# Performance work log

Measured on AMD Instinct MI355X. Metric: run time of the kernel, lower is better.

## Reference

```python
import jax, jax.numpy as jnp
import numpy as np
from jax import lax

FIELD = 32          # backbone receptive-field stride (field_size of ResNet50)
K = 3               # number of anchor sizes
ANCHOR_PX = (32, 64, 96)
POOL = 2
TILES = 3
NMS_IOU = 0.3
R_POST = 512        # post-NMS proposal cap (static shape for jit)
IMG = 1536
MG = IMG // FIELD   # 48x48 feature map
C = 256
HID = 1024


def setup_inputs() -> dict:
    key = jax.random.key(0)
    ks = jax.random.split(key, 6)
    # create_anchors: per feature cell (grid step FIELD) and per anchor size,
    # row = [x_upper_left, y_upper_left, width, height]
    grid = np.arange(MG, dtype=np.float32) * FIELD + FIELD / 2.0  # cell centers
    cy, cx, aa = np.meshgrid(grid, grid, np.array(ANCHOR_PX, np.float32), indexing='ij')
    anchors = np.stack([cx - aa / 2, cy - aa / 2, aa, aa], axis=-1).reshape(-1, 4).astype(np.float32)
    return {
        'features': jax.random.normal(ks[0], (1, MG, MG, C), jnp.float32),
        'anchors': jnp.asarray(anchors),
        'W_obj': jax.random.normal(ks[1], (C, 2 * K), jnp.float32) * 0.1,
        'b_obj': jnp.zeros((2 * K,), jnp.float32),
        'W_reg': jax.random.normal(ks[2], (C, 4 * K), jnp.float32) * 0.01,
        'b_reg': jnp.zeros((4 * K,), jnp.float32),
        'W_fc1': jax.random.normal(ks[3], (TILES * TILES * C, HID), jnp.float32) * 0.02,
        'b_fc1': jnp.zeros((HID,), jnp.float32),
        'W_fc2': jax.random.normal(ks[4], (HID, 4), jnp.float32) * 0.01,
        'b_fc2': jnp.zeros((4,), jnp.float32),
    }


def _map_outputs(out, anchors):
    # out: [M, N, K*D] RPN output; returns [A, D], one row per anchor
    apx = jnp.asarray(ANCHOR_PX, jnp.int32)
    k = jnp.argmax(anchors[:, 3].astype(jnp.int32)[:, None] == apx[None, :], axis=1)
    px = ((anchors[:, 0] + anchors[:, 2] * 0.5) / FIELD).astype(jnp.int32)
    py = ((anchors[:, 1] + anchors[:, 3] * 0.5) / FIELD).astype(jnp.int32)
    M, N, _ = out.shape
    r = out.reshape(M, N, K, -1)
    return r[py, px, k]


def _unparameterize(reg, anchors):
    cxa = anchors[:, 0] + anchors[:, 2] * 0.5
    cya = anchors[:, 1] + anchors[:, 3] * 0.5
    cx = reg[:, 0] * anchors[:, 2] + cxa
    cy = reg[:, 1] * anchors[:, 3] + cya
    w = anchors[:, 2] * jnp.exp(reg[:, 2])
    h = anchors[:, 3] * jnp.exp(reg[:, 3])
    return jnp.stack([cx - w * 0.5, cy - h * 0.5, w, h], axis=1)


def _clip_boxes(b, W, H):
    x1 = jnp.clip(b[:, 0], 0.0, W)
    y1 = jnp.clip(b[:, 1], 0.0, H)
    x2 = jnp.clip(b[:, 0] + b[:, 2], 0.0, W)
    y2 = jnp.clip(b[:, 1] + b[:, 3], 0.0, H)
    return jnp.stack([x1, y1, x2 - x1, y2 - y1], axis=1)


def _pairwise_iou(b):
    x1, y1 = b[:, 0], b[:, 1]
    x2, y2 = b[:, 0] + b[:, 2], b[:, 1] + b[:, 3]
    iw = jnp.maximum(0.0, jnp.minimum(x2[:, None], x2[None, :]) - jnp.maximum(x1[:, None], x1[None, :]))
    ih = jnp.maximum(0.0, jnp.minimum(y2[:, None], y2[None, :]) - jnp.maximum(y1[:, None], y1[None, :]))
    inter = iw * ih
    area = (x2 - x1) * (y2 - y1)
    return inter / (area[:, None] + area[None, :] - inter + 1e-8)


def _roialign(fmap, boxes):
    # fmap: [M, N, C]; boxes: [R, 4] xywh -> [R, TILES, TILES, C]
    M, N, Cc = fmap.shape
    S = TILES * POOL
    offs = (jnp.arange(S, dtype=boxes.dtype) + 0.5) / S
    fx = jnp.clip((boxes[:, 0:1] + offs[None, :] * boxes[:, 2:3]) / FIELD - 0.5, 0.0, N - 1.0)
    fy = jnp.clip((boxes[:, 1:2] + offs[None, :] * boxes[:, 3:4]) / FIELD - 0.5, 0.0, M - 1.0)
    x0 = jnp.floor(fx).astype(jnp.int32); x1 = jnp.minimum(x0 + 1, N - 1); wx = fx - x0
    y0 = jnp.floor(fy).astype(jnp.int32); y1 = jnp.minimum(y0 + 1, M - 1); wy = fy - y0
    def g(yi, xi):
        return fmap[yi[:, :, None], xi[:, None, :]]  # [R, S, S, C]
    wX = wx[:, None, :, None]; wY = wy[:, :, None, None]
    v = (g(y0, x0) * (1 - wY) * (1 - wX) + g(y0, x1) * (1 - wY) * wX
         + g(y1, x0) * wY * (1 - wX) + g(y1, x1) * wY * wX)
    R = boxes.shape[0]
    return v.reshape(R, TILES, POOL, TILES, POOL, Cc).mean(axis=(2, 4))


def reference(features, anchors, W_obj, b_obj, W_reg, b_reg, W_fc1, b_fc1, W_fc2, b_fc2):
    fmap = features[0]  # [M, N, C]
    out_obj = fmap @ W_obj + b_obj   # [M, N, 2K]
    out_reg = fmap @ W_reg + b_reg   # [M, N, 4K]
    rpn_obj = jax.nn.softmax(_map_outputs(out_obj, anchors), axis=1)  # [A, 2]
    rpn_reg = _map_outputs(out_reg, anchors)                          # [A, 4]
    boxes = _clip_boxes(_unparameterize(rpn_reg, anchors), float(IMG), float(IMG))
    scores = rpn_obj[:, 1]
    A = boxes.shape[0]
    # NMS (sequential greedy suppression on score-sorted boxes)
    order = jnp.argsort(-scores)
    iou_mat = lax.stop_gradient(_pairwise_iou(boxes[order]))  # [A, A], index selection is non-diff
    idx = jnp.arange(A)
    def body(i, keep):
        sup = jnp.any((iou_mat[i] > NMS_IOU) & keep & (idx < i))
        return keep.at[i].set(~sup)
    keep = lax.fori_loop(0, A, body, jnp.zeros((A,), bool))
    masked = jnp.where(keep, scores[order], -1e9)
    _, topi = lax.top_k(masked, R_POST)
    sel = order[topi]
    sel_boxes = boxes[sel]
    sel_obj = rpn_obj[sel]
    pooled = _roialign(fmap, sel_boxes)            # [R, TILES, TILES, C]
    flat = pooled.reshape(R_POST, -1)
    h = jax.nn.relu(flat @ W_fc1 + b_fc1)
    align_reg = h @ W_fc2 + b_fc2                  # [R, 4]
    align_boxes = _unparameterize(align_reg, sel_boxes)
    # concat (rpn_obj, rpn_boxes, align_boxes) -> [R, 10]
    return jnp.concatenate([sel_obj, sel_boxes, align_boxes], axis=1)
```

## Files before the change

### kernel.cpp

```cpp
#include <hip/hip_runtime.h>
#include <hip/hip_bf16.h>

typedef unsigned long long ull;

#define MGRID 48
#define CCH   256
#define NCELL 2304
#define NA    6912
#define NW    108
#define NHID  1024
#define KFC   2304
#define RPOST 512
#define IMGF  1536.0f

typedef __attribute__((ext_vector_type(8))) short short8v;
typedef __attribute__((ext_vector_type(4))) float f32x4;

__global__ __launch_bounds__(256) void rpn_wcvt(const float* __restrict__ feat,
    const float* __restrict__ Wobj, const float* __restrict__ bobj,
    const float* __restrict__ Wreg, const float* __restrict__ breg,
    float* __restrict__ rpn, const float* __restrict__ Wfc1,
    ushort* __restrict__ Wt){
  if (blockIdx.x >= 162){
    __shared__ float tile[32][33];
    int bid = blockIdx.x - 162;
    int bx = bid & 31;
    int by = bid >> 5;
    int tx = threadIdx.x & 31, ty = threadIdx.x >> 5;
    #pragma unroll
    for (int it=0; it<4; ++it)
      tile[ty + 8*it][tx] = Wfc1[(size_t)(by*32 + ty + 8*it)*NHID + bx*32 + tx];
    __syncthreads();
    #pragma unroll
    for (int it=0; it<4; ++it){
      __hip_bfloat16 b = __float2bfloat16(tile[tx][ty + 8*it]);
      Wt[(size_t)(bx*32 + ty + 8*it)*KFC + by*32 + tx] = *(ushort*)&b;
    }
    return;
  }
  int g = blockIdx.x*256 + threadIdx.x;
  int cell = g / 18, o = g % 18;
  const float* W; int stride; float acc;
  if (o < 6){ W = Wobj + o; stride = 6;  acc = bobj[o];   }
  else      { W = Wreg + (o-6); stride = 12; acc = breg[o-6]; }
  const float4* x4 = (const float4*)(feat + cell*CCH);
  #pragma unroll 4
  for (int c4=0;c4<CCH/4;++c4){
    float4 xv = x4[c4];
    acc += xv.x*W[(4*c4+0)*stride];
    acc += xv.y*W[(4*c4+1)*stride];
    acc += xv.z*W[(4*c4+2)*stride];
    acc += xv.w*W[(4*c4+3)*stride];
  }
  rpn[cell*18 + o] = acc;
}

__global__ __launch_bounds__(256) void anchor_prep(const float* __restrict__ rpn,
    const float* __restrict__ anchors, float* __restrict__ probs,
    float* __restrict__ boxes, ull* __restrict__ keys){
  int a = blockIdx.x*256 + threadIdx.x;
  int cell = a/3, k = a%3;
  const float* rc = rpn + cell*18;
  float l0 = rc[2*k], l1 = rc[2*k+1];
  float m  = fmaxf(l0,l1);
  float e0 = expf(l0-m), e1 = expf(l1-m);
  float s  = e0 + e1;
  float p0 = e0/s, p1 = e1/s;
  probs[a*2+0] = p0; probs[a*2+1] = p1;
  float4 an = ((const float4*)anchors)[a];
  float r0 = rc[6+4*k+0], r1 = rc[6+4*k+1], r2 = rc[6+4*k+2], r3 = rc[6+4*k+3];
  float cxa = an.x + an.z*0.5f, cya = an.y + an.w*0.5f;
  float cx = r0*an.z + cxa, cy = r1*an.w + cya;
  float w  = an.z*expf(r2),  hh = an.w*expf(r3);
  float bx = cx - w*0.5f, by = cy - hh*0.5f;
  float x1 = fminf(fmaxf(bx,      0.0f), IMGF);
  float y1 = fminf(fmaxf(by,      0.0f), IMGF);
  float x2 = fminf(fmaxf(bx + w,  0.0f), IMGF);
  float y2 = fminf(fmaxf(by + hh, 0.0f), IMGF);
  float4 bo; bo.x = x1; bo.y = y1; bo.z = x2 - x1; bo.w = y2 - y1;
  ((float4*)boxes)[a] = bo;
  keys[a] = ((ull)__float_as_uint(p1) << 32) | (unsigned)(NA-1-a);
}

__global__ __launch_bounds__(256) void rank_part(const ull* __restrict__ keys,
                                                 int* __restrict__ part){
  __shared__ ull lk[256];
  int t = threadIdx.x;
  int ib = blockIdx.x, jb = blockIdx.y;
  lk[t] = keys[jb*256 + t];
  int i = ib*256 + t;
  ull ki = keys[i];
  __syncthreads();
  int cnt = 0;
  #pragma unroll 16
  for (int j=0;j<256;++j) cnt += (lk[j] > ki) ? 1 : 0;
  part[jb*NA + i] = cnt;
}

__global__ __launch_bounds__(256) void rank_scatter(const int* __restrict__ part,
    const float* __restrict__ boxes, int* __restrict__ ord, float* __restrict__ sboxes){
  int i = blockIdx.x*256 + threadIdx.x;
  int r = 0;
  #pragma unroll
  for (int jb=0;jb<27;++jb) r += part[jb*NA + i];
  ord[r] = i;
  ((float4*)sboxes)[r] = ((const float4*)boxes)[i];
}

#define NQ 5993
__global__ __launch_bounds__(256) void iou_mask(const float* __restrict__ sboxes,
                                                ull* __restrict__ maskT){
  int g = blockIdx.x*256 + threadIdx.x;
  int q = g >> 6;
  if (q >= NQ) return;
  int w = (int)((sqrtf(8.0f*(float)q + 9.0f) - 3.0f) * 0.5f);
  if (w > 107) w = 107;
  while (w < 107 && (w+1)*(w+4)/2 <= q) ++w;
  while (w > 0 && w*(w+3)/2 > q) --w;
  int ib = q - w*(w+3)/2;
  int i = ib*64 + (g & 63);
  float4 bi = ((const float4*)sboxes)[i];
  float x1i = bi.x, y1i = bi.y;
  float x2i = bi.x + bi.z, y2i = bi.y + bi.w;
  float ai  = (x2i - x1i) * (y2i - y1i);
  const float4* bj4 = (const float4*)sboxes + w*64;
  ull bits = 0;
  #pragma unroll 8
  for (int jj=0;jj<64;++jj){
    float4 bj = bj4[jj];
    float x1j = bj.x, y1j = bj.y;
    float x2j = bj.x + bj.z, y2j = bj.y + bj.w;
    float aj  = (x2j - x1j) * (y2j - y1j);
    float iw = fmaxf(fminf(x2i,x2j) - fmaxf(x1i,x1j), 0.0f);
    float ih = fmaxf(fminf(y2i,y2j) - fmaxf(y1i,y1j), 0.0f);
    float inter = iw*ih;
    float den = ai + aj - inter + 1e-8f;
    if (inter > 0.3f*den) bits |= (1ull<<jj);
  }
  maskT[(size_t)w*NA + i] = bits;
}

__global__ __launch_bounds__(256) void nms(const ull* __restrict__ maskT,
    const int* __restrict__ ord, const float* __restrict__ sboxes,
    const float* __restrict__ probs, float* __restrict__ out,
    float* __restrict__ selb){
  __shared__ ull remv[NW];
  __shared__ ull keepw[NW];
  __shared__ ull kb_sh[2];
  __shared__ int selpos[RPOST];
  __shared__ int base_sh[NW];
  __shared__ int cnt_sh, done_sh;
  int t = threadIdx.x;
  if (t < NW){ remv[t] = 0ull; keepw[t] = 0ull; }
  if (t == 0){ cnt_sh = 0; done_sh = 0; kb_sh[0] = 0ull; kb_sh[1] = 0ull; }
  __syncthreads();

  ull dg_cur = 0, srow_cur = 0, kb_prev = 0;
  if (t < 64) dg_cur = maskT[t];

  for (int c = 0; c < NW; ++c){
    if (t < 64){
      ull dg_nxt = 0, srow_nxt = 0;
      if (c+1 < NW){
        dg_nxt   = maskT[(size_t)(c+1)*NA + (size_t)(c+1)*64 + t];
        srow_nxt = maskT[(size_t)c*NA + (size_t)(c+1)*64 + t];
      }
      ull w0 = remv[c];
      bool dec  = ((w0 >> t) & 1ull) || ((srow_cur & kb_prev) != 0ull);
      bool kept = false;
      ull sup = dg_cur & ((1ull << t) - 1ull);
      for (;;){
        ull K = __ballot(kept);
        ull D = __ballot(dec);
        if (D == ~0ull) break;
        if (!dec){
          if (sup & K)                 { dec = true; }
          else if ((sup & ~D) == 0ull) { dec = true; kept = true; }
        }
      }
      ull kb = __ballot(kept);
      int cnt0 = cnt_sh;
      ull below = kb & ((1ull << t) - 1ull);
      int myrank = cnt0 + __popcll(below);
      if (kept && myrank < RPOST) selpos[myrank] = c*64 + t;
      if (t == 0){
        kb_sh[c & 1] = kb;
        keepw[c] = kb;
        int nc = cnt0 + __popcll(kb);
        if (nc >= RPOST){ nc = RPOST; done_sh = 1; }
        cnt_sh = nc;
      }
      kb_prev = kb; dg_cur = dg_nxt; srow_cur = srow_nxt;
    } else {
      int u = t - 64;
      int wp = c + 1 + u;
      if (c >= 1 && wp < NW){
        ull kbp = kb_sh[(c-1) & 1];
        if (kbp){
          const ull* row = maskT + (size_t)wp*NA + (size_t)(c-1)*64;
          ull acc = remv[wp];
          #pragma unroll
          for (int b=0;b<64;++b)
            acc |= (0ull - ((kbp >> b) & 1ull)) & row[b];
          remv[wp] = acc;
        }
      }
    }
    __syncthreads();
    if (done_sh) break;
  }
  __syncthreads();
  int cnt0 = cnt_sh;
  if (cnt0 < RPOST){
    if (t < NW){
      int s = 0;
      for (int w2=0; w2<t; ++w2) s += __popcll(~keepw[w2]);
      base_sh[t] = s;
    }
    __syncthreads();
    for (int p = t; p < NA; p += 256){
      int w2 = p >> 6, b = p & 63;
      ull kw = keepw[w2];
      if (!((kw >> b) & 1ull)){
        int rank = cnt0 + base_sh[w2] + __popcll(~kw & ((1ull << b) - 1ull));
        if (rank < RPOST) selpos[rank] = p;
      }
    }
  }
  __syncthreads();
  for (int s=t; s<RPOST; s+=256){
    int pos = selpos[s];
    int orig = ord[pos];
    float4 b = ((const float4*)sboxes)[pos];
    out[s*10+0] = probs[orig*2+0];
    out[s*10+1] = probs[orig*2+1];
    out[s*10+2] = b.x; out[s*10+3] = b.y; out[s*10+4] = b.z; out[s*10+5] = b.w;
    ((float4*)selb)[s] = b;
  }
}

__global__ __launch_bounds__(256) void roialign(const float* __restrict__ feat,
    const float* __restrict__ selb, __hip_bfloat16* __restrict__ pooled){
  int r = blockIdx.x, c = threadIdx.x;
  float4 b = ((const float4*)selb)[r];
  int x0[6], x1[6], y0[6], y1[6];
  float wx[6], wy[6];
  #pragma unroll
  for (int s=0;s<6;++s){
    float off = ((float)s + 0.5f) / 6.0f;
    float fx = (b.x + off*b.z) / 32.0f - 0.5f;
    fx = fminf(fmaxf(fx, 0.0f), 47.0f);
    int xx0 = (int)floorf(fx);
    x0[s] = xx0; x1[s] = min(xx0+1, 47); wx[s] = fx - (float)xx0;
    float fy = (b.y + off*b.w) / 32.0f - 0.5f;
    fy = fminf(fmaxf(fy, 0.0f), 47.0f);
    int yy0 = (int)floorf(fy);
    y0[s] = yy0; y1[s] = min(yy0+1, 47); wy[s] = fy - (float)yy0;
  }
  #pragma unroll
  for (int ty=0;ty<3;++ty){
    #pragma unroll
    for (int tx=0;tx<3;++tx){
      float sum = 0.0f;
      #pragma unroll
      for (int py=0;py<2;++py){
        #pragma unroll
        for (int px=0;px<2;++px){
          int sy = ty*2+py, sx = tx*2+px;
          float wxx = wx[sx], wyy = wy[sy];
          float v00 = feat[(y0[sy]*MGRID + x0[sx])*CCH + c];
          float v01 = feat[(y0[sy]*MGRID + x1[sx])*CCH + c];
          float v10 = feat[(y1[sy]*MGRID + x0[sx])*CCH + c];
          float v11 = feat[(y1[sy]*MGRID + x1[sx])*CCH + c];
          sum += v00*(1.0f-wyy)*(1.0f-wxx) + v01*(1.0f-wyy)*wxx
               + v10*wyy*(1.0f-wxx)        + v11*wyy*wxx;
        }
      }
      pooled[((r*9) + ty*3 + tx)*CCH + c] = __float2bfloat16(sum * 0.25f);
    }
  }
}

__global__ __launch_bounds__(256) void fc1_mfma(const ushort* __restrict__ A,
    const ushort* __restrict__ Bt, const float* __restrict__ bias,
    float* __restrict__ Hp){
  __shared__ ushort As[4096];
  __shared__ ushort Bs[4096];
  const int t = threadIdx.x;
  const int bn = blockIdx.x, bm = blockIdx.y, bz = blockIdx.z;
  const int wv = t >> 6, lane = t & 63;
  const int wm = (wv >> 1) * 32, wn = (wv & 1) * 32;

  const int r0 = t >> 3, kc = t & 7;
  const int r1 = r0 + 32;
  const int kbase = bz * 144;
  const float4* gA0 = (const float4*)A  + (size_t)(bm*64 + r0)*288 + kbase + kc;
  const float4* gA1 = (const float4*)A  + (size_t)(bm*64 + r1)*288 + kbase + kc;
  const float4* gB0 = (const float4*)Bt + (size_t)(bn*64 + r0)*288 + kbase + kc;
  const float4* gB1 = (const float4*)Bt + (size_t)(bn*64 + r1)*288 + kbase + kc;
  float4* sA0 = (float4*)As + ((r0<<3) | (kc ^ (r0&7)));
  float4* sA1 = (float4*)As + ((r1<<3) | (kc ^ (r1&7)));
  float4* sB0 = (float4*)Bs + ((r0<<3) | (kc ^ (r0&7)));
  float4* sB1 = (float4*)Bs + ((r1<<3) | (kc ^ (r1&7)));

  const int fr = lane & 15, fkg = lane >> 4;
  const int arow0 = wm + fr,      arow1 = wm + 16 + fr;
  const int brow0 = wn + fr,      brow1 = wn + 16 + fr;

  f32x4 acc00{}, acc01{}, acc10{}, acc11{};

  const int KT = 18;
  float4 pa0 = gA0[0], pa1 = gA1[0], pb0 = gB0[0], pb1 = gB1[0];
  for (int kt = 0; kt < KT; ++kt){
    __syncthreads();
    *sA0 = pa0; *sA1 = pa1; *sB0 = pb0; *sB1 = pb1;
    if (kt + 1 < KT){
      pa0 = gA0[(kt+1)*8]; pa1 = gA1[(kt+1)*8];
      pb0 = gB0[(kt+1)*8]; pb1 = gB1[(kt+1)*8];
    }
    __syncthreads();
    #pragma unroll
    for (int kk2 = 0; kk2 < 2; ++kk2){
      int kidx = fkg + kk2*4;
      short8v a0 = *(const short8v*)(As + ((((arow0<<3) | (kidx ^ (arow0&7)))) << 3));
      short8v a1 = *(const short8v*)(As + ((((arow1<<3) | (kidx ^ (arow1&7)))) << 3));
      short8v b0 = *(const short8v*)(Bs + ((((brow0<<3) | (kidx ^ (brow0&7)))) << 3));
      short8v b1 = *(const short8v*)(Bs + ((((brow1<<3) | (kidx ^ (brow1&7)))) << 3));
      acc00 = __builtin_amdgcn_mfma_f32_16x16x32_bf16(a0, b0, acc00, 0, 0, 0);
      acc01 = __builtin_amdgcn_mfma_f32_16x16x32_bf16(a0, b1, acc01, 0, 0, 0);
      acc10 = __builtin_amdgcn_mfma_f32_16x16x32_bf16(a1, b0, acc10, 0, 0, 0);
      acc11 = __builtin_amdgcn_mfma_f32_16x16x32_bf16(a1, b1, acc11, 0, 0, 0);
    }
  }
  float* H = Hp + (size_t)bz * 512 * NHID;
  const int orow = bm*64 + wm + (lane>>4)*4;
  const int ocol = bn*64 + wn + (lane&15);
  #pragma unroll
  for (int i=0;i<2;++i){
    #pragma unroll
    for (int j=0;j<2;++j){
      f32x4 a = (i==0) ? ((j==0)?acc00:acc01) : ((j==0)?acc10:acc11);
      #pragma unroll
      for (int reg=0;reg<4;++reg){
        int row = orow + i*16 + reg;
        int col = ocol + j*16;
        float v = a[reg] + (bz == 0 ? bias[col] : 0.0f);
        H[(size_t)row*NHID + col] = v;
      }
    }
  }
}

__global__ __launch_bounds__(64) void fc2(const float* __restrict__ h0,
    const float* __restrict__ h1, const float* __restrict__ W2,
    const float* __restrict__ b2, const float* __restrict__ selb,
    float* __restrict__ out){
  int r = blockIdx.x, lane = threadIdx.x;
  float a0=0,a1=0,a2=0,a3=0;
  #pragma unroll 4
  for (int it=0; it<16; ++it){
    int k = it*64 + lane;
    float hv = fmaxf(h0[(size_t)r*NHID + k] + h1[(size_t)r*NHID + k], 0.0f);
    float4 w = ((const float4*)W2)[k];
    a0 += hv*w.x; a1 += hv*w.y; a2 += hv*w.z; a3 += hv*w.w;
  }
  #pragma unroll
  for (int off=32; off>0; off>>=1){
    a0 += __shfl_down(a0, off);
    a1 += __shfl_down(a1, off);
    a2 += __shfl_down(a2, off);
    a3 += __shfl_down(a3, off);
  }
  if (lane == 0){
    float4 b = ((const float4*)selb)[r];
    float r0 = a0 + b2[0], r1 = a1 + b2[1], r2 = a2 + b2[2], r3 = a3 + b2[3];
    float cxa = b.x + b.z*0.5f, cya = b.y + b.w*0.5f;
    float cx = r0*b.z + cxa, cy = r1*b.w + cya;
    float w  = b.z*expf(r2),  hh = b.w*expf(r3);
    out[r*10+6] = cx - w*0.5f;
    out[r*10+7] = cy - hh*0.5f;
    out[r*10+8] = w;
    out[r*10+9] = hh;
  }
}

extern "C" void kernel_launch(void* const* d_in, const int* in_sizes, int n_in,
                              void* d_out, int out_size, void* d_ws, size_t ws_size,
                              hipStream_t stream) {
  const float* feat    = (const float*)d_in[0];
  const float* anchors = (const float*)d_in[1];
  const float* Wobj    = (const float*)d_in[2];
  const float* bobj    = (const float*)d_in[3];
  const float* Wreg    = (const float*)d_in[4];
  const float* breg    = (const float*)d_in[5];
  const float* Wfc1    = (const float*)d_in[6];
  const float* bfc1    = (const float*)d_in[7];
  const float* Wfc2    = (const float*)d_in[8];
  const float* bfc2    = (const float*)d_in[9];
  float* out = (float*)d_out;
  char* ws = (char*)d_ws;

  float* rpn    = (float*)(ws + 0);
  float* probs  = (float*)(ws + 165888);
  float* boxes  = (float*)(ws + 221184);
  ull*   keys   = (ull*)  (ws + 331776);
  int*   ord    = (int*)  (ws + 387072);
  float* sboxes = (float*)(ws + 414720);
  int*   part   = (int*)  (ws + 525312);
  ull*   maskT  = (ull*)  (ws + 1271808);
  float* selb   = (float*)(ws + 7243776);
  __hip_bfloat16* pooled = (__hip_bfloat16*)(ws + 7251968);
  float* h      = (float*)(ws + 9611264);
  ushort* Wt    = (ushort*)(ws + 13805568);

  float* h0 = h;
  float* h1 = h + 512*NHID;

  hipLaunchKernelGGL(rpn_wcvt,     dim3(2466),    dim3(256), 0, stream, feat, Wobj, bobj, Wreg, breg, rpn, Wfc1, Wt);
  hipLaunchKernelGGL(anchor_prep,  dim3(27),      dim3(256), 0, stream, rpn, anchors, probs, boxes, keys);
  hipLaunchKernelGGL(rank_part,    dim3(27,27),   dim3(256), 0, stream, keys, part);
  hipLaunchKernelGGL(rank_scatter, dim3(27),      dim3(256), 0, stream, part, boxes, ord, sboxes);
  hipLaunchKernelGGL(iou_mask,     dim3(1499),    dim3(256), 0, stream, sboxes, maskT);
  hipLaunchKernelGGL(nms,          dim3(1),       dim3(256), 0, stream, maskT, ord, sboxes, probs, out, selb);
  hipLaunchKernelGGL(roialign,     dim3(512),     dim3(256), 0, stream, feat, selb, pooled);
  hipLaunchKernelGGL(fc1_mfma,     dim3(16,8,2),  dim3(256), 0, stream, (const ushort*)pooled, Wt, bfc1, h);
  hipLaunchKernelGGL(fc2,          dim3(512),     dim3(64),  0, stream, h0, h1, Wfc2, bfc2, selb, out);
}
```

Before: 91.21 us.

## Fuse pipeline into one persistent kernel with grid-wide atomic barriers

Replaces the nine separate kernel launches with a single persistent kernel of 256 blocks, using a counter-based grid barrier between stages, plus a small init kernel that resets the counters. Each stage loops over virtual blocks to cover its original grid. The goal is to remove the launch gaps and per-launch overhead between the many short stages. The NMS mask-row reads are also widened to 128-bit loads. The cost is that stages which previously ran on thousands of blocks are now confined to 256 blocks, the single-block NMS leaves the other blocks spinning, and correctness depends on all 256 blocks being co-resident.

```diff
diff --git a/kernel.cpp b/kernel.cpp
--- a/kernel.cpp
+++ b/kernel.cpp
@@ -12,375 +12,398 @@
 #define KFC   2304
 #define RPOST 512
 #define IMGF  1536.0f
+#define NBLK  256
+#define NQ    5993
 
 typedef __attribute__((ext_vector_type(8))) short short8v;
 typedef __attribute__((ext_vector_type(4))) float f32x4;
 
-__global__ __launch_bounds__(256) void rpn_wcvt(const float* __restrict__ feat,
+__device__ inline void gsync(unsigned* ctr, int slot){
+  __syncthreads();
+  if (threadIdx.x == 0){
+    __threadfence();
+    atomicAdd(&ctr[slot], 1u);
+    while (__hip_atomic_load(&ctr[slot], __ATOMIC_RELAXED, __HIP_MEMORY_SCOPE_AGENT) < NBLK)
+      __builtin_amdgcn_s_sleep(4);
+    __threadfence();
+  }
+  __syncthreads();
+}
+
+__global__ void init_sync(unsigned* c){ if (threadIdx.x < 16) c[threadIdx.x] = 0u; }
+
+__global__ __launch_bounds__(256) void fused(
+    const float* __restrict__ feat, const float* __restrict__ anchors,
     const float* __restrict__ Wobj, const float* __restrict__ bobj,
     const float* __restrict__ Wreg, const float* __restrict__ breg,
-    float* __restrict__ rpn, const float* __restrict__ Wfc1,
-    ushort* __restrict__ Wt){
-  if (blockIdx.x >= 162){
-    __shared__ float tile[32][33];
-    int bid = blockIdx.x - 162;
-    int bx = bid & 31;
-    int by = bid >> 5;
-    int tx = threadIdx.x & 31, ty = threadIdx.x >> 5;
+    const float* __restrict__ Wfc1, const float* __restrict__ bfc1,
+    const float* __restrict__ Wfc2, const float* __restrict__ bfc2,
+    float* __restrict__ rpn, float* __restrict__ probs, float* __restrict__ boxes,
+    ull* __restrict__ keys, int* __restrict__ ord, float* __restrict__ sboxes,
+    int* __restrict__ part, ull* __restrict__ maskT, float* __restrict__ selb,
+    ushort* __restrict__ pooled, float* __restrict__ h, ushort* __restrict__ Wt,
+    float* __restrict__ out, unsigned* __restrict__ sctr){
+  const int bid = blockIdx.x;
+  const int t   = threadIdx.x;
+
+  __shared__ float tile[32][33];
+  __shared__ ull  lk[256];
+  __shared__ ull  remv[NW], keepw[NW], kb_sh[2];
+  __shared__ int  selpos[RPOST], base_sh[NW];
+  __shared__ int  cnt_sh, done_sh;
+  __shared__ ushort As[4096], Bs[4096];
+
+  if (bid < 162){
+    int g = bid*256 + t;
+    int cell = g / 18, o = g % 18;
+    const float* W; int stride; float acc;
+    if (o < 6){ W = Wobj + o; stride = 6;  acc = bobj[o];   }
+    else      { W = Wreg + (o-6); stride = 12; acc = breg[o-6]; }
+    const float4* x4 = (const float4*)(feat + cell*CCH);
+    #pragma unroll 4
+    for (int c4=0;c4<CCH/4;++c4){
+      float4 xv = x4[c4];
+      acc += xv.x*W[(4*c4+0)*stride];
+      acc += xv.y*W[(4*c4+1)*stride];
+      acc += xv.z*W[(4*c4+2)*stride];
+      acc += xv.w*W[(4*c4+3)*stride];
+    }
+    rpn[cell*18 + o] = acc;
+  }
+  {
+    int tx = t & 31, ty = t >> 5;
+    for (int vb = bid; vb < 2304; vb += NBLK){
+      int bx = vb & 31, by = vb >> 5;
+      #pragma unroll
+      for (int it=0; it<4; ++it)
+        tile[ty + 8*it][tx] = Wfc1[(size_t)(by*32 + ty + 8*it)*NHID + bx*32 + tx];
+      __syncthreads();
+      #pragma unroll
+      for (int it=0; it<4; ++it){
+        __hip_bfloat16 b = __float2bfloat16(tile[tx][ty + 8*it]);
+        Wt[(size_t)(bx*32 + ty + 8*it)*KFC + by*32 + tx] = *(ushort*)&b;
+      }
+      __syncthreads();
+    }
+  }
+  gsync(sctr, 0);
+
+  {
+    int a = bid*256 + t;
+    if (a < NA){
+      int cell = a/3, k = a%3;
+      const float* rc = rpn + cell*18;
+      float l0 = rc[2*k], l1 = rc[2*k+1];
+      float m  = fmaxf(l0,l1);
+      float e0 = expf(l0-m), e1 = expf(l1-m);
+      float s  = e0 + e1;
+      float p0 = e0/s, p1 = e1/s;
+      probs[a*2+0] = p0; probs[a*2+1] = p1;
+      float4 an = ((const float4*)anchors)[a];
+      float r0 = rc[6+4*k+0], r1 = rc[6+4*k+1], r2 = rc[6+4*k+2], r3 = rc[6+4*k+3];
+      float cxa = an.x + an.z*0.5f, cya = an.y + an.w*0.5f;
+      float cx = r0*an.z + cxa, cy = r1*an.w + cya;
+      float w  = an.z*expf(r2),  hh = an.w*expf(r3);
+      float bx = cx - w*0.5f, by = cy - hh*0.5f;
+      float x1 = fminf(fmaxf(bx,      0.0f), IMGF);
+      float y1 = fminf(fmaxf(by,      0.0f), IMGF);
+      float x2 = fminf(fmaxf(bx + w,  0.0f), IMGF);
+      float y2 = fminf(fmaxf(by + hh, 0.0f), IMGF);
+      float4 bo; bo.x = x1; bo.y = y1; bo.z = x2 - x1; bo.w = y2 - y1;
+      ((float4*)boxes)[a] = bo;
+      keys[a] = ((ull)__float_as_uint(p1) << 32) | (unsigned)(NA-1-a);
+    }
+  }
+  gsync(sctr, 1);
+
+  for (int vb = bid; vb < 729; vb += NBLK){
+    int ib = vb % 27, jb = vb / 27;
+    __syncthreads();
+    lk[t] = keys[jb*256 + t];
+    int i = ib*256 + t;
+    ull ki = keys[i];
+    __syncthreads();
+    int cnt = 0;
+    #pragma unroll 16
+    for (int j=0;j<256;++j) cnt += (lk[j] > ki) ? 1 : 0;
+    part[jb*NA + i] = cnt;
+  }
+  gsync(sctr, 2);
+
+  if (bid < 27){
+    int i = bid*256 + t;
+    int r = 0;
     #pragma unroll
-    for (int it=0; it<4; ++it)
-      tile[ty + 8*it][tx] = Wfc1[(size_t)(by*32 + ty + 8*it)*NHID + bx*32 + tx];
+    for (int jb=0;jb<27;++jb) r += part[jb*NA + i];
+    ord[r] = i;
+    ((float4*)sboxes)[r] = ((const float4*)boxes)[i];
+  }
+  gsync(sctr, 3);
+
+  for (int vb = bid; vb < 1499; vb += NBLK){
+    int g = vb*256 + t;
+    int q = g >> 6;
+    if (q < NQ){
+      int w = (int)((sqrtf(8.0f*(float)q + 9.0f) - 3.0f) * 0.5f);
+      if (w > 107) w = 107;
+      while (w < 107 && (w+1)*(w+4)/2 <= q) ++w;
+      while (w > 0 && w*(w+3)/2 > q) --w;
+      int ib = q - w*(w+3)/2;
+      int i = ib*64 + (g & 63);
+      float4 bi = ((const float4*)sboxes)[i];
+      float x1i = bi.x, y1i = bi.y;
+      float x2i = bi.x + bi.z, y2i = bi.y + bi.w;
+      float ai  = (x2i - x1i) * (y2i - y1i);
+      const float4* bj4 = (const float4*)sboxes + w*64;
+      ull bits = 0;
+      #pragma unroll 8
+      for (int jj=0;jj<64;++jj){
+        float4 bj = bj4[jj];
+        float x1j = bj.x, y1j = bj.y;
+        float x2j = bj.x + bj.z, y2j = bj.y + bj.w;
+        float aj  = (x2j - x1j) * (y2j - y1j);
+        float iw = fmaxf(fminf(x2i,x2j) - fmaxf(x1i,x1j), 0.0f);
+        float ih = fmaxf(fminf(y2i,y2j) - fmaxf(y1i,y1j), 0.0f);
+        float inter = iw*ih;
+        float den = ai + aj - inter + 1e-8f;
+        if (inter > 0.3f*den) bits |= (1ull<<jj);
+      }
+      maskT[(size_t)w*NA + i] = bits;
+    }
+  }
+  gsync(sctr, 4);
+
+  if (bid == 0){
+    if (t < NW){ remv[t] = 0ull; keepw[t] = 0ull; }
+    if (t == 0){ cnt_sh = 0; done_sh = 0; kb_sh[0] = 0ull; kb_sh[1] = 0ull; }
     __syncthreads();
+
+    ull dg_cur = 0, srow_cur = 0, kb_prev = 0;
+    if (t < 64) dg_cur = maskT[t];
+
+    for (int c = 0; c < NW; ++c){
+      if (t < 64){
+        ull dg_nxt = 0, srow_nxt = 0;
+        if (c+1 < NW){
+          dg_nxt   = maskT[(size_t)(c+1)*NA + (size_t)(c+1)*64 + t];
+          srow_nxt = maskT[(size_t)c*NA + (size_t)(c+1)*64 + t];
+        }
+        ull w0 = remv[c];
+        bool dec  = ((w0 >> t) & 1ull) || ((srow_cur & kb_prev) != 0ull);
+        bool kept = false;
+        ull sup = dg_cur & ((1ull << t) - 1ull);
+        for (;;){
+          ull K = __ballot(kept);
+          ull D = __ballot(dec);
+          if (D == ~0ull) break;
+          if (!dec){
+            if (sup & K)                 { dec = true; }
+            else if ((sup & ~D) == 0ull) { dec = true; kept = true; }
+          }
+        }
+        ull kb = __ballot(kept);
+        int cnt0 = cnt_sh;
+        ull below = kb & ((1ull << t) - 1ull);
+        int myrank = cnt0 + __popcll(below);
+        if (kept && myrank < RPOST) selpos[myrank] = c*64 + t;
+        if (t == 0){
+          kb_sh[c & 1] = kb;
+          keepw[c] = kb;
+          int nc = cnt0 + __popcll(kb);
+          if (nc >= RPOST){ nc = RPOST; done_sh = 1; }
+          cnt_sh = nc;
+        }
+        kb_prev = kb; dg_cur = dg_nxt; srow_cur = srow_nxt;
+      } else {
+        int u = t - 64;
+        int wp = c + 1 + u;
+        if (c >= 1 && wp < NW){
+          ull kbp = kb_sh[(c-1) & 1];
+          if (kbp){
+            const ulonglong2* row2 = (const ulonglong2*)(maskT + (size_t)wp*NA + (size_t)(c-1)*64);
+            ull acc = remv[wp];
+            #pragma unroll
+            for (int b=0;b<32;++b){
+              ulonglong2 v = row2[b];
+              acc |= (0ull - ((kbp >> (2*b))   & 1ull)) & v.x;
+              acc |= (0ull - ((kbp >> (2*b+1)) & 1ull)) & v.y;
+            }
+            remv[wp] = acc;
+          }
+        }
+      }
+      __syncthreads();
+      if (done_sh) break;
+    }
+    __syncthreads();
+    int cnt0 = cnt_sh;
+    if (cnt0 < RPOST){
+      if (t < NW){
+        int s = 0;
+        for (int w2=0; w2<t; ++w2) s += __popcll(~keepw[w2]);
+        base_sh[t] = s;
+      }
+      __syncthreads();
+      for (int p = t; p < NA; p += 256){
+        int w2 = p >> 6, b = p & 63;
+        ull kw = keepw[w2];
+        if (!((kw >> b) & 1ull)){
+          int rank = cnt0 + base_sh[w2] + __popcll(~kw & ((1ull << b) - 1ull));
+          if (rank < RPOST) selpos[rank] = p;
+        }
+      }
+    }
+    __syncthreads();
+    for (int s=t; s<RPOST; s+=256){
+      int pos = selpos[s];
+      int orig = ord[pos];
+      float4 b = ((const float4*)sboxes)[pos];
+      out[s*10+0] = probs[orig*2+0];
+      out[s*10+1] = probs[orig*2+1];
+      out[s*10+2] = b.x; out[s*10+3] = b.y; out[s*10+4] = b.z; out[s*10+5] = b.w;
+      ((float4*)selb)[s] = b;
+    }
+  }
+  gsync(sctr, 5);
+
+  for (int r = bid; r < RPOST; r += NBLK){
+    float4 b = ((const float4*)selb)[r];
+    int x0[6], x1[6], y0[6], y1[6];
+    float wx[6], wy[6];
     #pragma unroll
-    for (int it=0; it<4; ++it){
-      __hip_bfloat16 b = __float2bfloat16(tile[tx][ty + 8*it]);
-      Wt[(size_t)(bx*32 + ty + 8*it)*KFC + by*32 + tx] = *(ushort*)&b;
-    }
-    return;
-  }
-  int g = blockIdx.x*256 + threadIdx.x;
-  int cell = g / 18, o = g % 18;
-  const float* W; int stride; float acc;
-  if (o < 6){ W = Wobj + o; stride = 6;  acc = bobj[o];   }
-  else      { W = Wreg + (o-6); stride = 12; acc = breg[o-6]; }
-  const float4* x4 = (const float4*)(feat + cell*CCH);
-  #pragma unroll 4
-  for (int c4=0;c4<CCH/4;++c4){
-    float4 xv = x4[c4];
-    acc += xv.x*W[(4*c4+0)*stride];
-    acc += xv.y*W[(4*c4+1)*stride];
-    acc += xv.z*W[(4*c4+2)*stride];
-    acc += xv.w*W[(4*c4+3)*stride];
-  }
-  rpn[cell*18 + o] = acc;
-}
-
-__global__ __launch_bounds__(256) void anchor_prep(const float* __restrict__ rpn,
-    const float* __restrict__ anchors, float* __restrict__ probs,
-    float* __restrict__ boxes, ull* __restrict__ keys){
-  int a = blockIdx.x*256 + threadIdx.x;
-  int cell = a/3, k = a%3;
-  const float* rc = rpn + cell*18;
-  float l0 = rc[2*k], l1 = rc[2*k+1];
-  float m  = fmaxf(l0,l1);
-  float e0 = expf(l0-m), e1 = expf(l1-m);
-  float s  = e0 + e1;
-  float p0 = e0/s, p1 = e1/s;
-  probs[a*2+0] = p0; probs[a*2+1] = p1;
-  float4 an = ((const float4*)anchors)[a];
-  float r0 = rc[6+4*k+0], r1 = rc[6+4*k+1], r2 = rc[6+4*k+2], r3 = rc[6+4*k+3];
-  float cxa = an.x + an.z*0.5f, cya = an.y + an.w*0.5f;
-  float cx = r0*an.z + cxa, cy = r1*an.w + cya;
-  float w  = an.z*expf(r2),  hh = an.w*expf(r3);
-  float bx = cx - w*0.5f, by = cy - hh*0.5f;
-  float x1 = fminf(fmaxf(bx,      0.0f), IMGF);
-  float y1 = fminf(fmaxf(by,      0.0f), IMGF);
-  float x2 = fminf(fmaxf(bx + w,  0.0f), IMGF);
-  float y2 = fminf(fmaxf(by + hh, 0.0f), IMGF);
-  float4 bo; bo.x = x1; bo.y = y1; bo.z = x2 - x1; bo.w = y2 - y1;
-  ((float4*)boxes)[a] = bo;
-  keys[a] = ((ull)__float_as_uint(p1) << 32) | (unsigned)(NA-1-a);
-}
-
-__global__ __launch_bounds__(256) void rank_part(const ull* __restrict__ keys,
-                                                 int* __restrict__ part){
-  __shared__ ull lk[256];
-  int t = threadIdx.x;
-  int ib = blockIdx.x, jb = blockIdx.y;
-  lk[t] = keys[jb*256 + t];
-  int i = ib*256 + t;
-  ull ki = keys[i];
-  __syncthreads();
-  int cnt = 0;
-  #pragma unroll 16
-  for (int j=0;j<256;++j) cnt += (lk[j] > ki) ? 1 : 0;
-  part[jb*NA + i] = cnt;
-}
-
-__global__ __launch_bounds__(256) void rank_scatter(const int* __restrict__ part,
-    const float* __restrict__ boxes, int* __restrict__ ord, float* __restrict__ sboxes){
-  int i = blockIdx.x*256 + threadIdx.x;
-  int r = 0;
-  #pragma unroll
-  for (int jb=0;jb<27;++jb) r += part[jb*NA + i];
-  ord[r] = i;
-  ((float4*)sboxes)[r] = ((const float4*)boxes)[i];
-}
-
-#define NQ 5993
-__global__ __launch_bounds__(256) void iou_mask(const float* __restrict__ sboxes,
-                                                ull* __restrict__ maskT){
-  int g = blockIdx.x*256 + threadIdx.x;
-  int q = g >> 6;
-  if (q >= NQ) return;
-  int w = (int)((sqrtf(8.0f*(float)q + 9.0f) - 3.0f) * 0.5f);
-  if (w > 107) w = 107;
-  while (w < 107 && (w+1)*(w+4)/2 <= q) ++w;
-  while (w > 0 && w*(w+3)/2 > q) --w;
-  int ib = q - w*(w+3)/2;
-  int i = ib*64 + (g & 63);
-  float4 bi = ((const float4*)sboxes)[i];
-  float x1i = bi.x, y1i = bi.y;
-  float x2i = bi.x + bi.z, y2i = bi.y + bi.w;
-  float ai  = (x2i - x1i) * (y2i - y1i);
-  const float4* bj4 = (const float4*)sboxes + w*64;
-  ull bits = 0;
-  #pragma unroll 8
-  for (int jj=0;jj<64;++jj){
-    float4 bj = bj4[jj];
-    float x1j = bj.x, y1j = bj.y;
-    float x2j = bj.x + bj.z, y2j = bj.y + bj.w;
-    float aj  = (x2j - x1j) * (y2j - y1j);
-    float iw = fmaxf(fminf(x2i,x2j) - fmaxf(x1i,x1j), 0.0f);
-    float ih = fmaxf(fminf(y2i,y2j) - fmaxf(y1i,y1j), 0.0f);
-    float inter = iw*ih;
-    float den = ai + aj - inter + 1e-8f;
-    if (inter > 0.3f*den) bits |= (1ull<<jj);
-  }
-  maskT[(size_t)w*NA + i] = bits;
-}
-
-__global__ __launch_bounds__(256) void nms(const ull* __restrict__ maskT,
-    const int* __restrict__ ord, const float* __restrict__ sboxes,
-    const float* __restrict__ probs, float* __restrict__ out,
-    float* __restrict__ selb){
-  __shared__ ull remv[NW];
-  __shared__ ull keepw[NW];
-  __shared__ ull kb_sh[2];
-  __shared__ int selpos[RPOST];
-  __shared__ int base_sh[NW];
-  __shared__ int cnt_sh, done_sh;
-  int t = threadIdx.x;
-  if (t < NW){ remv[t] = 0ull; keepw[t] = 0ull; }
-  if (t == 0){ cnt_sh = 0; done_sh = 0; kb_sh[0] = 0ull; kb_sh[1] = 0ull; }
-  __syncthreads();
-
-  ull dg_cur = 0, srow_cur = 0, kb_prev = 0;
-  if (t < 64) dg_cur = maskT[t];
-
-  for (int c = 0; c < NW; ++c){
-    if (t < 64){
-      ull dg_nxt = 0, srow_nxt = 0;
-      if (c+1 < NW){
-        dg_nxt   = maskT[(size_t)(c+1)*NA + (size_t)(c+1)*64 + t];
-        srow_nxt = maskT[(size_t)c*NA + (size_t)(c+1)*64 + t];
-      }
-      ull w0 = remv[c];
-      bool dec  = ((w0 >> t) & 1ull) || ((srow_cur & kb_prev) != 0ull);
-      bool kept = false;
-      ull sup = dg_cur & ((1ull << t) - 1ull);
-      for (;;){
-        ull K = __ballot(kept);
-        ull D = __ballot(dec);
-        if (D == ~0ull) break;
-        if (!dec){
-          if (sup & K)                 { dec = true; }
-          else if ((sup & ~D) == 0ull) { dec = true; kept = true; }
-        }
-      }
-      ull kb = __ballot(kept);
-      int cnt0 = cnt_sh;
-      ull below = kb & ((1ull << t) - 1ull);
-      int myrank = cnt0 + __popcll(below);
-      if (kept && myrank < RPOST) selpos[myrank] = c*64 + t;
-      if (t == 0){
-        kb_sh[c & 1] = kb;
-        keepw[c] = kb;
-        int nc = cnt0 + __popcll(kb);
-        if (nc >= RPOST){ nc = RPOST; done_sh = 1; }
-        cnt_sh = nc;
-      }
-      kb_prev = kb; dg_cur = dg_nxt; srow_cur = srow_nxt;
-    } else {
-      int u = t - 64;
-      int wp = c + 1 + u;
-      if (c >= 1 && wp < NW){
-        ull kbp = kb_sh[(c-1) & 1];
-        if (kbp){
-          const ull* row = maskT + (size_t)wp*NA + (size_t)(c-1)*64;
-          ull acc = remv[wp];
+    for (int s=0;s<6;++s){
+      float off = ((float)s + 0.5f) / 6.0f;
+      float fx = (b.x + off*b.z) / 32.0f - 0.5f;
+      fx = fminf(fmaxf(fx, 0.0f), 47.0f);
+      int xx0 = (int)floorf(fx);
+      x0[s] = xx0; x1[s] = min(xx0+1, 47); wx[s] = fx - (float)xx0;
+      float fy = (b.y + off*b.w) / 32.0f - 0.5f;
+      fy = fminf(fmaxf(fy, 0.0f), 47.0f);
+      int yy0 = (int)floorf(fy);
+      y0[s] = yy0; y1[s] = min(yy0+1, 47); wy[s] = fy - (float)yy0;
+    }
+    int c = t;
+    #pragma unroll
+    for (int ty=0;ty<3;++ty){
+      #pragma unroll
+      for (int tx=0;tx<3;++tx){
+        float sum = 0.0f;
+        #pragma unroll
+        for (int py=0;py<2;++py){
           #pragma unroll
-          for (int b=0;b<64;++b)
-            acc |= (0ull - ((kbp >> b) & 1ull)) & row[b];
-          remv[wp] = acc;
-        }
-      }
-    }
-    __syncthreads();
-    if (done_sh) break;
-  }
-  __syncthreads();
-  int cnt0 = cnt_sh;
-  if (cnt0 < RPOST){
-    if (t < NW){
-      int s = 0;
-      for (int w2=0; w2<t; ++w2) s += __popcll(~keepw[w2]);
-      base_sh[t] = s;
-    }
-    __syncthreads();
-    for (int p = t; p < NA; p += 256){
-      int w2 = p >> 6, b = p & 63;
-      ull kw = keepw[w2];
-      if (!((kw >> b) & 1ull)){
-        int rank = cnt0 + base_sh[w2] + __popcll(~kw & ((1ull << b) - 1ull));
-        if (rank < RPOST) selpos[rank] = p;
-      }
-    }
-  }
-  __syncthreads();
-  for (int s=t; s<RPOST; s+=256){
-    int pos = selpos[s];
-    int orig = ord[pos];
-    float4 b = ((const float4*)sboxes)[pos];
-    out[s*10+0] = probs[orig*2+0];
-    out[s*10+1] = probs[orig*2+1];
-    out[s*10+2] = b.x; out[s*10+3] = b.y; out[s*10+4] = b.z; out[s*10+5] = b.w;
-    ((float4*)selb)[s] = b;
-  }
-}
-
-__global__ __launch_bounds__(256) void roialign(const float* __restrict__ feat,
-    const float* __restrict__ selb, __hip_bfloat16* __restrict__ pooled){
-  int r = blockIdx.x, c = threadIdx.x;
-  float4 b = ((const float4*)selb)[r];
-  int x0[6], x1[6], y0[6], y1[6];
-  float wx[6], wy[6];
-  #pragma unroll
-  for (int s=0;s<6;++s){
-    float off = ((float)s + 0.5f) / 6.0f;
-    float fx = (b.x + off*b.z) / 32.0f - 0.5f;
-    fx = fminf(fmaxf(fx, 0.0f), 47.0f);
-    int xx0 = (int)floorf(fx);
-    x0[s] = xx0; x1[s] = min(xx0+1, 47); wx[s] = fx - (float)xx0;
-    float fy = (b.y + off*b.w) / 32.0f - 0.5f;
-    fy = fminf(fmaxf(fy, 0.0f), 47.0f);
-    int yy0 = (int)floorf(fy);
-    y0[s] = yy0; y1[s] = min(yy0+1, 47); wy[s] = fy - (float)yy0;
-  }
-  #pragma unroll
-  for (int ty=0;ty<3;++ty){
+          for (int px=0;px<2;++px){
+            int sy = ty*2+py, sx = tx*2+px;
+            float wxx = wx[sx], wyy = wy[sy];
+            float v00 = feat[(y0[sy]*MGRID + x0[sx])*CCH + c];
+            float v01 = feat[(y0[sy]*MGRID + x1[sx])*CCH + c];
+            float v10 = feat[(y1[sy]*MGRID + x0[sx])*CCH + c];
+            float v11 = feat[(y1[sy]*MGRID + x1[sx])*CCH + c];
+            sum += v00*(1.0f-wyy)*(1.0f-wxx) + v01*(1.0f-wyy)*wxx
+                 + v10*wyy*(1.0f-wxx)        + v11*wyy*wxx;
+          }
+        }
+        __hip_bfloat16 pb = __float2bfloat16(sum * 0.25f);
+        pooled[((r*9) + ty*3 + tx)*CCH + c] = *(ushort*)&pb;
+      }
+    }
+  }
+  gsync(sctr, 6);
+
+  {
+    const int bn = bid & 15, bm = (bid >> 4) & 7, bz = bid >> 7;
+    const int wv = t >> 6, lane = t & 63;
+    const int wm = (wv >> 1) * 32, wn = (wv & 1) * 32;
+    const int r0 = t >> 3, kc = t & 7;
+    const int r1 = r0 + 32;
+    const int kbase = bz * 144;
+    const float4* gA0 = (const float4*)pooled + (size_t)(bm*64 + r0)*288 + kbase + kc;
+    const float4* gA1 = (const float4*)pooled + (size_t)(bm*64 + r1)*288 + kbase + kc;
+    const float4* gB0 = (const float4*)Wt     + (size_t)(bn*64 + r0)*288 + kbase + kc;
+    const float4* gB1 = (const float4*)Wt     + (size_t)(bn*64 + r1)*288 + kbase + kc;
+    float4* sA0 = (float4*)As + ((r0<<3) | (kc ^ (r0&7)));
+    float4* sA1 = (float4*)As + ((r1<<3) | (kc ^ (r1&7)));
+    float4* sB0 = (float4*)Bs + ((r0<<3) | (kc ^ (r0&7)));
+    float4* sB1 = (float4*)Bs + ((r1<<3) | (kc ^ (r1&7)));
+    const int fr = lane & 15, fkg = lane >> 4;
+    const int arow0 = wm + fr,  arow1 = wm + 16 + fr;
+    const int brow0 = wn + fr,  brow1 = wn + 16 + fr;
+    f32x4 acc00{}, acc01{}, acc10{}, acc11{};
+    const int KT = 18;
+    float4 pa0 = gA0[0], pa1 = gA1[0], pb0 = gB0[0], pb1 = gB1[0];
+    for (int kt = 0; kt < KT; ++kt){
+      __syncthreads();
+      *sA0 = pa0; *sA1 = pa1; *sB0 = pb0; *sB1 = pb1;
+      if (kt + 1 < KT){
+        pa0 = gA0[(kt+1)*8]; pa1 = gA1[(kt+1)*8];
+        pb0 = gB0[(kt+1)*8]; pb1 = gB1[(kt+1)*8];
+      }
+      __syncthreads();
+      #pragma unroll
+      for (int kk2 = 0; kk2 < 2; ++kk2){
+        int kidx = fkg + kk2*4;
+        short8v a0 = *(const short8v*)(As + ((((arow0<<3) | (kidx ^ (arow0&7)))) << 3));
+        short8v a1 = *(const short8v*)(As + ((((arow1<<3) | (kidx ^ (arow1&7)))) << 3));
+        short8v b0 = *(const short8v*)(Bs + ((((brow0<<3) | (kidx ^ (brow0&7)))) << 3));
+        short8v b1 = *(const short8v*)(Bs + ((((brow1<<3) | (kidx ^ (brow1&7)))) << 3));
+        acc00 = __builtin_amdgcn_mfma_f32_16x16x32_bf16(a0, b0, acc00, 0, 0, 0);
+        acc01 = __builtin_amdgcn_mfma_f32_16x16x32_bf16(a0, b1, acc01, 0, 0, 0);
+        acc10 = __builtin_amdgcn_mfma_f32_16x16x32_bf16(a1, b0, acc10, 0, 0, 0);
+        acc11 = __builtin_amdgcn_mfma_f32_16x16x32_bf16(a1, b1, acc11, 0, 0, 0);
+      }
+    }
+    float* H = h + (size_t)bz * 512 * NHID;
+    const int orow = bm*64 + wm + (lane>>4)*4;
+    const int ocol = bn*64 + wn + (lane&15);
     #pragma unroll
-    for (int tx=0;tx<3;++tx){
-      float sum = 0.0f;
-      #pragma unroll
-      for (int py=0;py<2;++py){
+    for (int i=0;i<2;++i){
+      #pragma unroll
+      for (int j=0;j<2;++j){
+        f32x4 a = (i==0) ? ((j==0)?acc00:acc01) : ((j==0)?acc10:acc11);
         #pragma unroll
-        for (int px=0;px<2;++px){
-          int sy = ty*2+py, sx = tx*2+px;
-          float wxx = wx[sx], wyy = wy[sy];
-          float v00 = feat[(y0[sy]*MGRID + x0[sx])*CCH + c];
-          float v01 = feat[(y0[sy]*MGRID + x1[sx])*CCH + c];
-          float v10 = feat[(y1[sy]*MGRID + x0[sx])*CCH + c];
-          float v11 = feat[(y1[sy]*MGRID + x1[sx])*CCH + c];
-          sum += v00*(1.0f-wyy)*(1.0f-wxx) + v01*(1.0f-wyy)*wxx
-               + v10*wyy*(1.0f-wxx)        + v11*wyy*wxx;
-        }
-      }
-      pooled[((r*9) + ty*3 + tx)*CCH + c] = __float2bfloat16(sum * 0.25f);
-    }
-  }
-}
-
-__global__ __launch_bounds__(256) void fc1_mfma(const ushort* __restrict__ A,
-    const ushort* __restrict__ Bt, const float* __restrict__ bias,
-    float* __restrict__ Hp){
-  __shared__ ushort As[4096];
-  __shared__ ushort Bs[4096];
-  const int t = threadIdx.x;
-  const int bn = blockIdx.x, bm = blockIdx.y, bz = blockIdx.z;
-  const int wv = t >> 6, lane = t & 63;
-  const int wm = (wv >> 1) * 32, wn = (wv & 1) * 32;
-
-  const int r0 = t >> 3, kc = t & 7;
-  const int r1 = r0 + 32;
-  const int kbase = bz * 144;
-  const float4* gA0 = (const float4*)A  + (size_t)(bm*64 + r0)*288 + kbase + kc;
-  const float4* gA1 = (const float4*)A  + (size_t)(bm*64 + r1)*288 + kbase + kc;
-  const float4* gB0 = (const float4*)Bt + (size_t)(bn*64 + r0)*288 + kbase + kc;
-  const float4* gB1 = (const float4*)Bt + (size_t)(bn*64 + r1)*288 + kbase + kc;
-  float4* sA0 = (float4*)As + ((r0<<3) | (kc ^ (r0&7)));
-  float4* sA1 = (float4*)As + ((r1<<3) | (kc ^ (r1&7)));
-  float4* sB0 = (float4*)Bs + ((r0<<3) | (kc ^ (r0&7)));
-  float4* sB1 = (float4*)Bs + ((r1<<3) | (kc ^ (r1&7)));
-
-  const int fr = lane & 15, fkg = lane >> 4;
-  const int arow0 = wm + fr,      arow1 = wm + 16 + fr;
-  const int brow0 = wn + fr,      brow1 = wn + 16 + fr;
-
-  f32x4 acc00{}, acc01{}, acc10{}, acc11{};
-
-  const int KT = 18;
-  float4 pa0 = gA0[0], pa1 = gA1[0], pb0 = gB0[0], pb1 = gB1[0];
-  for (int kt = 0; kt < KT; ++kt){
-    __syncthreads();
-    *sA0 = pa0; *sA1 = pa1; *sB0 = pb0; *sB1 = pb1;
-    if (kt + 1 < KT){
-      pa0 = gA0[(kt+1)*8]; pa1 = gA1[(kt+1)*8];
-      pb0 = gB0[(kt+1)*8]; pb1 = gB1[(kt+1)*8];
-    }
-    __syncthreads();
-    #pragma unroll
-    for (int kk2 = 0; kk2 < 2; ++kk2){
-      int kidx = fkg + kk2*4;
-      short8v a0 = *(const short8v*)(As + ((((arow0<<3) | (kidx ^ (arow0&7)))) << 3));
-      short8v a1 = *(const short8v*)(As + ((((arow1<<3) | (kidx ^ (arow1&7)))) << 3));
-      short8v b0 = *(const short8v*)(Bs + ((((brow0<<3) | (kidx ^ (brow0&7)))) << 3));
-      short8v b1 = *(const short8v*)(Bs + ((((brow1<<3) | (kidx ^ (brow1&7)))) << 3));
-      acc00 = __builtin_amdgcn_mfma_f32_16x16x32_bf16(a0, b0, acc00, 0, 0, 0);
-      acc01 = __builtin_amdgcn_mfma_f32_16x16x32_bf16(a0, b1, acc01, 0, 0, 0);
-      acc10 = __builtin_amdgcn_mfma_f32_16x16x32_bf16(a1, b0, acc10, 0, 0, 0);
-      acc11 = __builtin_amdgcn_mfma_f32_16x16x32_bf16(a1, b1, acc11, 0, 0, 0);
-    }
-  }
-  float* H = Hp + (size_t)bz * 512 * NHID;
-  const int orow = bm*64 + wm + (lane>>4)*4;
-  const int ocol = bn*64 + wn + (lane&15);
-  #pragma unroll
-  for (int i=0;i<2;++i){
-    #pragma unroll
-    for (int j=0;j<2;++j){
-      f32x4 a = (i==0) ? ((j==0)?acc00:acc01) : ((j==0)?acc10:acc11);
-      #pragma unroll
-      for (int reg=0;reg<4;++reg){
-        int row = orow + i*16 + reg;
-        int col = ocol + j*16;
-        float v = a[reg] + (bz == 0 ? bias[col] : 0.0f);
-        H[(size_t)row*NHID + col] = v;
-      }
-    }
-  }
-}
-
-__global__ __launch_bounds__(64) void fc2(const float* __restrict__ h0,
-    const float* __restrict__ h1, const float* __restrict__ W2,
-    const float* __restrict__ b2, const float* __restrict__ selb,
-    float* __restrict__ out){
-  int r = blockIdx.x, lane = threadIdx.x;
-  float a0=0,a1=0,a2=0,a3=0;
-  #pragma unroll 4
-  for (int it=0; it<16; ++it){
-    int k = it*64 + lane;
-    float hv = fmaxf(h0[(size_t)r*NHID + k] + h1[(size_t)r*NHID + k], 0.0f);
-    float4 w = ((const float4*)W2)[k];
-    a0 += hv*w.x; a1 += hv*w.y; a2 += hv*w.z; a3 += hv*w.w;
-  }
-  #pragma unroll
-  for (int off=32; off>0; off>>=1){
-    a0 += __shfl_down(a0, off);
-    a1 += __shfl_down(a1, off);
-    a2 += __shfl_down(a2, off);
-    a3 += __shfl_down(a3, off);
-  }
-  if (lane == 0){
-    float4 b = ((const float4*)selb)[r];
-    float r0 = a0 + b2[0], r1 = a1 + b2[1], r2 = a2 + b2[2], r3 = a3 + b2[3];
-    float cxa = b.x + b.z*0.5f, cya = b.y + b.w*0.5f;
-    float cx = r0*b.z + cxa, cy = r1*b.w + cya;
-    float w  = b.z*expf(r2),  hh = b.w*expf(r3);
-    out[r*10+6] = cx - w*0.5f;
-    out[r*10+7] = cy - hh*0.5f;
-    out[r*10+8] = w;
-    out[r*10+9] = hh;
+        for (int reg=0;reg<4;++reg){
+          int row = orow + i*16 + reg;
+          int col = ocol + j*16;
+          float v = a[reg] + (bz == 0 ? bfc1[col] : 0.0f);
+          H[(size_t)row*NHID + col] = v;
+        }
+      }
+    }
+  }
+  gsync(sctr, 7);
+
+  {
+    const float* h0 = h;
+    const float* h1 = h + 512*NHID;
+    int wv = t >> 6, lane = t & 63;
+    int r = bid*4 + wv;
+    if (r < RPOST){
+      float a0=0,a1=0,a2=0,a3=0;
+      #pragma unroll 4
+      for (int it=0; it<16; ++it){
+        int k = it*64 + lane;
+        float hv = fmaxf(h0[(size_t)r*NHID + k] + h1[(size_t)r*NHID + k], 0.0f);
+        float4 w = ((const float4*)Wfc2)[k];
+        a0 += hv*w.x; a1 += hv*w.y; a2 += hv*w.z; a3 += hv*w.w;
+      }
+      #pragma unroll
+      for (int off=32; off>0; off>>=1){
+        a0 += __shfl_down(a0, off);
+        a1 += __shfl_down(a1, off);
+        a2 += __shfl_down(a2, off);
+        a3 += __shfl_down(a3, off);
+      }
+      if (lane == 0){
+        float4 b = ((const float4*)selb)[r];
+        float r0 = a0 + bfc2[0], r1 = a1 + bfc2[1], r2 = a2 + bfc2[2], r3 = a3 + bfc2[3];
+        float cxa = b.x + b.z*0.5f, cya = b.y + b.w*0.5f;
+        float cx = r0*b.z + cxa, cy = r1*b.w + cya;
+        float w  = b.z*expf(r2),  hh = b.w*expf(r3);
+        out[r*10+6] = cx - w*0.5f;
+        out[r*10+7] = cy - hh*0.5f;
+        out[r*10+8] = w;
+        out[r*10+9] = hh;
+      }
+    }
   }
 }
 
@@ -409,20 +432,14 @@
   int*   part   = (int*)  (ws + 525312);
   ull*   maskT  = (ull*)  (ws + 1271808);
   float* selb   = (float*)(ws + 7243776);
-  __hip_bfloat16* pooled = (__hip_bfloat16*)(ws + 7251968);
+  ushort* pooled= (ushort*)(ws + 7251968);
   float* h      = (float*)(ws + 9611264);
   ushort* Wt    = (ushort*)(ws + 13805568);
-
-  float* h0 = h;
-  float* h1 = h + 512*NHID;
-
-  hipLaunchKernelGGL(rpn_wcvt,     dim3(2466),    dim3(256), 0, stream, feat, Wobj, bobj, Wreg, breg, rpn, Wfc1, Wt);
-  hipLaunchKernelGGL(anchor_prep,  dim3(27),      dim3(256), 0, stream, rpn, anchors, probs, boxes, keys);
-  hipLaunchKernelGGL(rank_part,    dim3(27,27),   dim3(256), 0, stream, keys, part);
-  hipLaunchKernelGGL(rank_scatter, dim3(27),      dim3(256), 0, stream, part, boxes, ord, sboxes);
-  hipLaunchKernelGGL(iou_mask,     dim3(1499),    dim3(256), 0, stream, sboxes, maskT);
-  hipLaunchKernelGGL(nms,          dim3(1),       dim3(256), 0, stream, maskT, ord, sboxes, probs, out, selb);
-  hipLaunchKernelGGL(roialign,     dim3(512),     dim3(256), 0, stream, feat, selb, pooled);
-  hipLaunchKernelGGL(fc1_mfma,     dim3(16,8,2),  dim3(256), 0, stream, (const ushort*)pooled, Wt, bfc1, h);
-  hipLaunchKernelGGL(fc2,          dim3(512),     dim3(64),  0, stream, h0, h1, Wfc2, bfc2, selb, out);
+  unsigned* sctr= (unsigned*)(ws + 18524160);
+
+  hipLaunchKernelGGL(init_sync, dim3(1),    dim3(64),  0, stream, sctr);
+  hipLaunchKernelGGL(fused,     dim3(NBLK), dim3(256), 0, stream,
+                     feat, anchors, Wobj, bobj, Wreg, breg, Wfc1, bfc1, Wfc2, bfc2,
+                     rpn, probs, boxes, keys, ord, sboxes, part, maskT, selb,
+                     pooled, h, Wt, out, sctr);
 }
```

Result: slower. 259.3 us (+184.3%).
